# Kernel tuning notes

Measured on AMD Instinct MI355X. Metric: run time of the kernel, lower is better.

Reference implementation:

```python
import jax, jax.numpy as jnp
import numpy as np

D_MODEL = 1024
NUM_HEADS = 16
HEAD_DIM = D_MODEL // NUM_HEADS
B, S = 2, 2048


def setup_inputs() -> dict:
    key = jax.random.key(0)
    ks = jax.random.split(key, 6)
    scale = 0.02
    return {
        "x": jax.random.normal(ks[0], (B, S, D_MODEL), dtype=jnp.float32),
        "mask": jax.random.normal(ks[1], (S, S), dtype=jnp.float32),
        "Wqkv": jax.random.normal(ks[2], (D_MODEL, 3 * D_MODEL), dtype=jnp.float32) * scale,
        "bqkv": jax.random.normal(ks[3], (3 * D_MODEL,), dtype=jnp.float32) * scale,
        "Wout": jax.random.normal(ks[4], (D_MODEL, D_MODEL), dtype=jnp.float32) * scale,
        "bout": jax.random.normal(ks[5], (D_MODEL,), dtype=jnp.float32) * scale,
    }


def reference(x, mask, Wqkv, bqkv, Wout, bout):
    b, s, d = x.shape
    h, hd = NUM_HEADS, HEAD_DIM
    qkv = x @ Wqkv + bqkv                              # [b, s, 3d]
    qkv = qkv.reshape(b, s, h, 3 * hd).transpose(0, 2, 1, 3)  # [b, h, s, 3hd]
    q, k, v = jnp.split(qkv, 3, axis=-1)               # each [b, h, s, hd]
    scaled = jnp.einsum("bhqd,bhkd->bhqk", q, k) / jnp.sqrt(jnp.float32(hd))
    scaled = scaled + mask                             # mask [s, s] broadcasts
    attn = jax.nn.softmax(scaled, axis=-1)
    values = jnp.einsum("bhqk,bhkd->bhqd", attn, v)    # [b, h, s, hd]
    values = values.transpose(0, 2, 1, 3).reshape(b, s, d)
    return values @ Wout + bout
```

## Files before the change

### kernel.cpp

```cpp
#include <hip/hip_runtime.h>
#include <hip/hip_bf16.h>

#define D_MODEL 1024
#define NH 16
#define HD 64
#define BATCH 2
#define SEQ 2048
#define M_TOTAL (BATCH*SEQ)

typedef _Float16 f16;
typedef _Float16 half8 __attribute__((ext_vector_type(8)));
typedef _Float16 half4v __attribute__((ext_vector_type(4)));
typedef float floatx4 __attribute__((ext_vector_type(4)));

__device__ inline void gload_lds16(const void* g, void* l) {
    __builtin_amdgcn_global_load_lds(
        (const __attribute__((address_space(1))) unsigned int*)g,
        (__attribute__((address_space(3))) unsigned int*)l, 16, 0, 0);
}

__global__ void cvt_f32_f16(const float* __restrict__ src, f16* __restrict__ dst, int n4) {
    int i = blockIdx.x * blockDim.x + threadIdx.x;
    if (i < n4) {
        float4 v = ((const float4*)src)[i];
        half4v o = { (f16)v.x, (f16)v.y, (f16)v.z, (f16)v.w };
        *(half4v*)(dst + (long)i * 4) = o;
    }
}

__global__ void exp_cvt(const float* __restrict__ src, f16* __restrict__ dst, int n4) {
    int i = blockIdx.x * blockDim.x + threadIdx.x;
    if (i < n4) {
        float4 v = ((const float4*)src)[i];
        half4v o = { (f16)__expf(v.x), (f16)__expf(v.y), (f16)__expf(v.z), (f16)__expf(v.w) };
        *(half4v*)(dst + (long)i * 4) = o;
    }
}

__global__ void transpose_cvt(const float* __restrict__ src, f16* __restrict__ dst, int R, int C) {
    __shared__ float tile[32][33];
    int tx = threadIdx.x;
    int ty = threadIdx.y;
    int c0 = blockIdx.x * 32;
    int r0 = blockIdx.y * 32;
    for (int yy = 0; yy < 32; yy += 8)
        tile[ty + yy][tx] = src[(long)(r0 + ty + yy) * C + c0 + tx];
    __syncthreads();
    for (int yy = 0; yy < 32; yy += 8)
        dst[(long)(c0 + ty + yy) * R + r0 + tx] = (f16)tile[tx][ty + yy];
}

template<int MODE, int TN>
__global__ __launch_bounds__(256) void gemm_mfma(
    const f16* __restrict__ A, const f16* __restrict__ BT,
    const float* __restrict__ bias,
    f16* __restrict__ Qh, f16* __restrict__ Kh, f16* __restrict__ Vtg,
    float* __restrict__ out, int Kdim)
{
    constexpr int NF = TN / 32;
    __shared__ f16 Ah[128 * 64];
    __shared__ f16 Bh[TN * 64];
    int tid  = threadIdx.x;
    int wid  = tid >> 6;
    int lane = tid & 63;
    int quad = lane >> 4;
    int l16  = lane & 15;
    int m0 = blockIdx.y * 128;
    int n0 = blockIdx.x * TN;
    int mrow = (wid >> 1) * 64;
    int ncol = (wid & 1) * (TN / 2);
    int grow = lane >> 3;
    int gchunk = (lane & 7) ^ (grow & 7);
    int sw0 = ((quad)     ^ (l16 & 7)) * 8;
    int sw1 = ((quad + 4) ^ (l16 & 7)) * 8;

    floatx4 acc[4][NF];
    #pragma unroll
    for (int mb = 0; mb < 4; mb++)
        #pragma unroll
        for (int nb = 0; nb < NF; nb++) acc[mb][nb] = (floatx4){0.f, 0.f, 0.f, 0.f};

    const f16* Abase = A + (long)m0 * Kdim;
    const f16* Bbase = BT + (long)n0 * Kdim;

    for (int k0 = 0; k0 < Kdim; k0 += 64) {
        #pragma unroll
        for (int j = 0; j < 4; j++) {
            int r = j * 32 + wid * 8 + grow;
            gload_lds16(Abase + (long)r * Kdim + k0 + gchunk * 8, &Ah[(j * 32 + wid * 8) * 64]);
        }
        #pragma unroll
        for (int j = 0; j < TN / 32; j++) {
            int r = j * 32 + wid * 8 + grow;
            gload_lds16(Bbase + (long)r * Kdim + k0 + gchunk * 8, &Bh[(j * 32 + wid * 8) * 64]);
        }
        __syncthreads();
        #pragma unroll
        for (int h = 0; h < 2; h++) {
            int sw = h ? sw1 : sw0;
            half8 af[4];
            #pragma unroll
            for (int mb = 0; mb < 4; mb++)
                af[mb] = *(const half8*)&Ah[(mrow + mb * 16 + l16) * 64 + sw];
            #pragma unroll
            for (int nb = 0; nb < NF; nb++) {
                half8 bf = *(const half8*)&Bh[(ncol + nb * 16 + l16) * 64 + sw];
                #pragma unroll
                for (int mb = 0; mb < 4; mb++)
                    acc[mb][nb] = __builtin_amdgcn_mfma_f32_16x16x32_f16(af[mb], bf, acc[mb][nb], 0, 0, 0);
            }
        }
        __syncthreads();
    }

    #pragma unroll
    for (int nb = 0; nb < NF; nb++) {
        int n = n0 + ncol + nb * 16 + l16;
        float bv = bias[n];
        int head = 0, t = 0, d = 0;
        if (MODE == 0) { head = n / 192; int rem = n % 192; t = rem / 64; d = rem % 64; }
        #pragma unroll
        for (int mb = 0; mb < 4; mb++) {
            int mbase = m0 + mrow + mb * 16 + quad * 4;
            if (MODE == 0) {
                int b = mbase >> 11;
                int s = mbase & 2047;
                long bh = b * NH + head;
                if (t == 2) {
                    half4v pack;
                    #pragma unroll
                    for (int r = 0; r < 4; r++) pack[r] = (f16)(acc[mb][nb][r] + bv);
                    *(half4v*)&Vtg[(bh * HD + d) * SEQ + s] = pack;
                } else if (t == 0) {
                    #pragma unroll
                    for (int r = 0; r < 4; r++)
                        Qh[(bh * SEQ + s + r) * HD + d] = (f16)((acc[mb][nb][r] + bv) * 0.125f);
                } else {
                    #pragma unroll
                    for (int r = 0; r < 4; r++)
                        Kh[(bh * SEQ + s + r) * HD + d] = (f16)(acc[mb][nb][r] + bv);
                }
            } else {
                #pragma unroll
                for (int r = 0; r < 4; r++)
                    out[(long)(mbase + r) * D_MODEL + n] = acc[mb][nb][r] + bv;
            }
        }
    }
}

__global__ __launch_bounds__(256) void attn(
    const f16* __restrict__ Qh, const f16* __restrict__ Kh, const f16* __restrict__ Vtg,
    const f16* __restrict__ E, f16* __restrict__ valh)
{
    __shared__ f16 Kl[2][64 * 64];
    __shared__ f16 Vt[2][64 * 64];
    __shared__ f16 Pl[4][32 * 64];
    int tid  = threadIdx.x;
    int wid  = tid >> 6;
    int lane = tid & 63;
    int quad = lane >> 4;
    int l16  = lane & 15;
    int bh = blockIdx.y;
    int b  = bh >> 4;
    int h  = bh & 15;
    int q0 = blockIdx.x * 128 + wid * 32;

    int grow = lane >> 3;
    int gpos = lane & 7;
    int sw0 = ((quad)     ^ (l16 & 7)) * 8;
    int sw1 = ((quad + 4) ^ (l16 & 7)) * 8;

    const f16* Qbase = Qh + ((long)bh * SEQ + q0) * HD;
    half8 qf[2][2];
    #pragma unroll
    for (int m = 0; m < 2; m++)
        #pragma unroll
        for (int c = 0; c < 2; c++)
            qf[m][c] = *(const half8*)&Qbase[(long)(m * 16 + l16) * HD + c * 32 + quad * 8];

    half8 vones;
    #pragma unroll
    for (int j = 0; j < 8; j++) vones[j] = (f16)1.0f;

    floatx4 Of[2][4];
    floatx4 Ofs[2];
    #pragma unroll
    for (int m = 0; m < 2; m++) {
        Ofs[m] = (floatx4){0.f, 0.f, 0.f, 0.f};
        #pragma unroll
        for (int nb = 0; nb < 4; nb++) Of[m][nb] = (floatx4){0.f, 0.f, 0.f, 0.f};
    }

    const f16* Kb = Kh + (long)bh * SEQ * HD;
    const f16* Vb = Vtg + (long)bh * HD * SEQ;

    #pragma unroll
    for (int j = 0; j < 2; j++) {
        int rb = j * 32 + wid * 8;
        int row = rb + grow;
        int gk = gpos ^ (row & 7);
        gload_lds16(Kb + (long)row * HD + gk * 8, &Kl[0][rb * 64]);
        gload_lds16(Vb + (long)row * SEQ + gk * 8, &Vt[0][rb * 64]);
    }

    for (int it = 0; it < SEQ / 64; it++) {
        int cur = it & 1;
        int k0 = it * 64;
        __syncthreads();

        if (it < SEQ / 64 - 1) {
            int kn = k0 + 64;
            #pragma unroll
            for (int j = 0; j < 2; j++) {
                int rb = j * 32 + wid * 8;
                int row = rb + grow;
                int gk = gpos ^ (row & 7);
                gload_lds16(Kb + (long)(kn + row) * HD + gk * 8, &Kl[cur ^ 1][rb * 64]);
                gload_lds16(Vb + (long)row * SEQ + kn + gk * 8, &Vt[cur ^ 1][rb * 64]);
            }
        }

        half4v ef[2][4];
        #pragma unroll
        for (int m = 0; m < 2; m++)
            #pragma unroll
            for (int kb = 0; kb < 4; kb++)
                ef[m][kb] = *(const half4v*)&E[(long)(q0 + m * 16 + l16) * SEQ + k0 + kb * 16 + quad * 4];

        #pragma unroll
        for (int kb = 0; kb < 4; kb++) {
            half8 kf0 = *(const half8*)&Kl[cur][(kb * 16 + l16) * 64 + sw0];
            half8 kf1 = *(const half8*)&Kl[cur][(kb * 16 + l16) * 64 + sw1];
            #pragma unroll
            for (int m = 0; m < 2; m++) {
                floatx4 s = (floatx4){0.f, 0.f, 0.f, 0.f};
                s = __builtin_amdgcn_mfma_f32_16x16x32_f16(kf0, qf[m][0], s, 0, 0, 0);
                s = __builtin_amdgcn_mfma_f32_16x16x32_f16(kf1, qf[m][1], s, 0, 0, 0);
                half4v ph;
                #pragma unroll
                for (int r = 0; r < 4; r++)
                    ph[r] = (f16)((float)ef[m][kb][r] * __expf(s[r]));
                int c8 = ((kb * 2 + (quad >> 1)) ^ (l16 & 7)) * 8 + (quad & 1) * 4;
                *(half4v*)&Pl[wid][(m * 16 + l16) * 64 + c8] = ph;
            }
        }

        half8 pf[2][2];
        #pragma unroll
        for (int m = 0; m < 2; m++)
            #pragma unroll
            for (int c = 0; c < 2; c++) {
                int c8 = ((c * 4 + quad) ^ (l16 & 7)) * 8;
                pf[m][c] = *(const half8*)&Pl[wid][(m * 16 + l16) * 64 + c8];
            }

        #pragma unroll
        for (int nb = 0; nb < 4; nb++) {
            half8 vf0 = *(const half8*)&Vt[cur][(nb * 16 + l16) * 64 + sw0];
            half8 vf1 = *(const half8*)&Vt[cur][(nb * 16 + l16) * 64 + sw1];
            #pragma unroll
            for (int m = 0; m < 2; m++) {
                Of[m][nb] = __builtin_amdgcn_mfma_f32_16x16x32_f16(pf[m][0], vf0, Of[m][nb], 0, 0, 0);
                Of[m][nb] = __builtin_amdgcn_mfma_f32_16x16x32_f16(pf[m][1], vf1, Of[m][nb], 0, 0, 0);
            }
        }
        #pragma unroll
        for (int m = 0; m < 2; m++) {
            Ofs[m] = __builtin_amdgcn_mfma_f32_16x16x32_f16(pf[m][0], vones, Ofs[m], 0, 0, 0);
            Ofs[m] = __builtin_amdgcn_mfma_f32_16x16x32_f16(pf[m][1], vones, Ofs[m], 0, 0, 0);
        }
    }

    #pragma unroll
    for (int m = 0; m < 2; m++) {
        floatx4 rs;
        #pragma unroll
        for (int r = 0; r < 4; r++) rs[r] = 1.f / Ofs[m][r];
        #pragma unroll
        for (int nb = 0; nb < 4; nb++)
            #pragma unroll
            for (int r = 0; r < 4; r++) {
                int q = q0 + m * 16 + quad * 4 + r;
                int d = nb * 16 + l16;
                valh[((long)(b * SEQ + q)) * D_MODEL + h * HD + d] = (f16)(Of[m][nb][r] * rs[r]);
            }
    }
}

extern "C" void kernel_launch(void* const* d_in, const int* in_sizes, int n_in,
                              void* d_out, int out_size, void* d_ws, size_t ws_size,
                              hipStream_t stream) {
    const float* x    = (const float*)d_in[0];
    const float* mask = (const float*)d_in[1];
    const float* Wqkv = (const float*)d_in[2];
    const float* bqkv = (const float*)d_in[3];
    const float* Wout = (const float*)d_in[4];
    const float* bout = (const float*)d_in[5];
    float* out = (float*)d_out;

    char* ws = (char*)d_ws;
    f16* xh    = (f16*)(ws + 0);
    f16* E     = (f16*)(ws + 0);
    f16* WqkvT = (f16*)(ws + 8388608);
    f16* WoutT = (f16*)(ws + 14680064);
    f16* Qh    = (f16*)(ws + 16777216);
    f16* Kh    = (f16*)(ws + 25165824);
    f16* Vtg   = (f16*)(ws + 33554432);
    f16* valh  = (f16*)(ws + 41943040);

    cvt_f32_f16<<<4096, 256, 0, stream>>>(x, xh, M_TOTAL * D_MODEL / 4);
    transpose_cvt<<<dim3(96, 32), dim3(32, 8), 0, stream>>>(Wqkv, WqkvT, 1024, 3072);
    transpose_cvt<<<dim3(32, 32), dim3(32, 8), 0, stream>>>(Wout, WoutT, 1024, 1024);
    gemm_mfma<0, 128><<<dim3(24, 32), 256, 0, stream>>>(xh, WqkvT, bqkv, Qh, Kh, Vtg, nullptr, 1024);
    exp_cvt<<<4096, 256, 0, stream>>>(mask, E, SEQ * SEQ / 4);
    attn<<<dim3(16, 32), 256, 0, stream>>>(Qh, Kh, Vtg, E, valh);
    gemm_mfma<1, 64><<<dim3(16, 32), 256, 0, stream>>>(valh, WoutT, bout, nullptr, nullptr, nullptr, out, 1024);
}
```

Before: 259.1 us.

## Keep P in registers, feed PV via 16x16x16 MFMA, prefetch mask

Result: faster. 243.3 us (-6.1%).

```diff
diff --git a/kernel.cpp b/kernel.cpp
--- a/kernel.cpp
+++ b/kernel.cpp
@@ -155,7 +155,6 @@
 {
     __shared__ f16 Kl[2][64 * 64];
     __shared__ f16 Vt[2][64 * 64];
-    __shared__ f16 Pl[4][32 * 64];
     int tid  = threadIdx.x;
     int wid  = tid >> 6;
     int lane = tid & 63;
@@ -168,8 +167,11 @@
 
     int grow = lane >> 3;
     int gpos = lane & 7;
-    int sw0 = ((quad)     ^ (l16 & 7)) * 8;
-    int sw1 = ((quad + 4) ^ (l16 & 7)) * 8;
+    int l3   = l16 & 7;
+    int sw0 = ((quad)     ^ l3) * 8;
+    int sw1 = ((quad + 4) ^ l3) * 8;
+    int qh  = quad >> 1;
+    int ql4 = (quad & 1) * 4;
 
     const f16* Qbase = Qh + ((long)bh * SEQ + q0) * HD;
     half8 qf[2][2];
@@ -179,18 +181,12 @@
         for (int c = 0; c < 2; c++)
             qf[m][c] = *(const half8*)&Qbase[(long)(m * 16 + l16) * HD + c * 32 + quad * 8];
 
-    half8 vones;
-    #pragma unroll
-    for (int j = 0; j < 8; j++) vones[j] = (f16)1.0f;
-
     floatx4 Of[2][4];
-    floatx4 Ofs[2];
-    #pragma unroll
-    for (int m = 0; m < 2; m++) {
-        Ofs[m] = (floatx4){0.f, 0.f, 0.f, 0.f};
+    float sums[2] = {0.f, 0.f};
+    #pragma unroll
+    for (int m = 0; m < 2; m++)
         #pragma unroll
         for (int nb = 0; nb < 4; nb++) Of[m][nb] = (floatx4){0.f, 0.f, 0.f, 0.f};
-    }
 
     const f16* Kb = Kh + (long)bh * SEQ * HD;
     const f16* Vb = Vtg + (long)bh * HD * SEQ;
@@ -204,87 +200,87 @@
         gload_lds16(Vb + (long)row * SEQ + gk * 8, &Vt[0][rb * 64]);
     }
 
-    for (int it = 0; it < SEQ / 64; it++) {
-        int cur = it & 1;
-        int k0 = it * 64;
-        __syncthreads();
-
-        if (it < SEQ / 64 - 1) {
-            int kn = k0 + 64;
-            #pragma unroll
-            for (int j = 0; j < 2; j++) {
-                int rb = j * 32 + wid * 8;
-                int row = rb + grow;
-                int gk = gpos ^ (row & 7);
-                gload_lds16(Kb + (long)(kn + row) * HD + gk * 8, &Kl[cur ^ 1][rb * 64]);
-                gload_lds16(Vb + (long)row * SEQ + kn + gk * 8, &Vt[cur ^ 1][rb * 64]);
-            }
-        }
-
-        half4v ef[2][4];
-        #pragma unroll
-        for (int m = 0; m < 2; m++)
-            #pragma unroll
-            for (int kb = 0; kb < 4; kb++)
-                ef[m][kb] = *(const half4v*)&E[(long)(q0 + m * 16 + l16) * SEQ + k0 + kb * 16 + quad * 4];
-
-        #pragma unroll
-        for (int kb = 0; kb < 4; kb++) {
-            half8 kf0 = *(const half8*)&Kl[cur][(kb * 16 + l16) * 64 + sw0];
-            half8 kf1 = *(const half8*)&Kl[cur][(kb * 16 + l16) * 64 + sw1];
-            #pragma unroll
-            for (int m = 0; m < 2; m++) {
-                floatx4 s = (floatx4){0.f, 0.f, 0.f, 0.f};
-                s = __builtin_amdgcn_mfma_f32_16x16x32_f16(kf0, qf[m][0], s, 0, 0, 0);
-                s = __builtin_amdgcn_mfma_f32_16x16x32_f16(kf1, qf[m][1], s, 0, 0, 0);
-                half4v ph;
-                #pragma unroll
-                for (int r = 0; r < 4; r++)
-                    ph[r] = (f16)((float)ef[m][kb][r] * __expf(s[r]));
-                int c8 = ((kb * 2 + (quad >> 1)) ^ (l16 & 7)) * 8 + (quad & 1) * 4;
-                *(half4v*)&Pl[wid][(m * 16 + l16) * 64 + c8] = ph;
-            }
-        }
-
-        half8 pf[2][2];
-        #pragma unroll
-        for (int m = 0; m < 2; m++)
-            #pragma unroll
-            for (int c = 0; c < 2; c++) {
-                int c8 = ((c * 4 + quad) ^ (l16 & 7)) * 8;
-                pf[m][c] = *(const half8*)&Pl[wid][(m * 16 + l16) * 64 + c8];
-            }
-
+    half4v ef[2][2][4];
+    #pragma unroll
+    for (int m = 0; m < 2; m++)
+        #pragma unroll
+        for (int kb = 0; kb < 4; kb++)
+            ef[0][m][kb] = *(const half4v*)&E[(long)(q0 + m * 16 + l16) * SEQ + kb * 16 + quad * 4];
+
+    for (int it2 = 0; it2 < SEQ / 128; it2++) {
+        #pragma unroll
+        for (int p = 0; p < 2; p++) {
+            int k0 = it2 * 128 + p * 64;
+            __syncthreads();
+
+            if (k0 + 64 < SEQ) {
+                int kn = k0 + 64;
+                #pragma unroll
+                for (int j = 0; j < 2; j++) {
+                    int rb = j * 32 + wid * 8;
+                    int row = rb + grow;
+                    int gk = gpos ^ (row & 7);
+                    gload_lds16(Kb + (long)(kn + row) * HD + gk * 8, &Kl[p ^ 1][rb * 64]);
+                    gload_lds16(Vb + (long)row * SEQ + kn + gk * 8, &Vt[p ^ 1][rb * 64]);
+                }
+                #pragma unroll
+                for (int m = 0; m < 2; m++)
+                    #pragma unroll
+                    for (int kb = 0; kb < 4; kb++)
+                        ef[p ^ 1][m][kb] = *(const half4v*)&E[(long)(q0 + m * 16 + l16) * SEQ + kn + kb * 16 + quad * 4];
+            }
+
+            half4v ph[2][4];
+            #pragma unroll
+            for (int kb = 0; kb < 4; kb++) {
+                half8 kf0 = *(const half8*)&Kl[p][(kb * 16 + l16) * 64 + sw0];
+                half8 kf1 = *(const half8*)&Kl[p][(kb * 16 + l16) * 64 + sw1];
+                #pragma unroll
+                for (int m = 0; m < 2; m++) {
+                    floatx4 s = (floatx4){0.f, 0.f, 0.f, 0.f};
+                    s = __builtin_amdgcn_mfma_f32_16x16x32_f16(kf0, qf[m][0], s, 0, 0, 0);
+                    s = __builtin_amdgcn_mfma_f32_16x16x32_f16(kf1, qf[m][1], s, 0, 0, 0);
+                    #pragma unroll
+                    for (int r = 0; r < 4; r++) {
+                        float pv = (float)ef[p][m][kb][r] * __expf(s[r]);
+                        sums[m] += pv;
+                        ph[m][kb][r] = (f16)pv;
+                    }
+                }
+            }
+
+            #pragma unroll
+            for (int kb = 0; kb < 4; kb++) {
+                int chunk = ((kb * 2 + qh) ^ l3) * 8 + ql4;
+                #pragma unroll
+                for (int nb = 0; nb < 4; nb++) {
+                    half4v vf = *(const half4v*)&Vt[p][(nb * 16 + l16) * 64 + chunk];
+                    #pragma unroll
+                    for (int m = 0; m < 2; m++)
+                        Of[m][nb] = __builtin_amdgcn_mfma_f32_16x16x16f16(vf, ph[m][kb], Of[m][nb], 0, 0, 0);
+                }
+            }
+        }
+    }
+
+    #pragma unroll
+    for (int m = 0; m < 2; m++) {
+        float s = sums[m];
+        s += __shfl_xor(s, 16);
+        s += __shfl_xor(s, 32);
+        sums[m] = 1.f / s;
+    }
+
+    #pragma unroll
+    for (int m = 0; m < 2; m++) {
+        long row = (long)(b * SEQ + q0 + m * 16 + l16) * D_MODEL + h * HD;
         #pragma unroll
         for (int nb = 0; nb < 4; nb++) {
-            half8 vf0 = *(const half8*)&Vt[cur][(nb * 16 + l16) * 64 + sw0];
-            half8 vf1 = *(const half8*)&Vt[cur][(nb * 16 + l16) * 64 + sw1];
-            #pragma unroll
-            for (int m = 0; m < 2; m++) {
-                Of[m][nb] = __builtin_amdgcn_mfma_f32_16x16x32_f16(pf[m][0], vf0, Of[m][nb], 0, 0, 0);
-                Of[m][nb] = __builtin_amdgcn_mfma_f32_16x16x32_f16(pf[m][1], vf1, Of[m][nb], 0, 0, 0);
-            }
-        }
-        #pragma unroll
-        for (int m = 0; m < 2; m++) {
-            Ofs[m] = __builtin_amdgcn_mfma_f32_16x16x32_f16(pf[m][0], vones, Ofs[m], 0, 0, 0);
-            Ofs[m] = __builtin_amdgcn_mfma_f32_16x16x32_f16(pf[m][1], vones, Ofs[m], 0, 0, 0);
-        }
-    }
-
-    #pragma unroll
-    for (int m = 0; m < 2; m++) {
-        floatx4 rs;
-        #pragma unroll
-        for (int r = 0; r < 4; r++) rs[r] = 1.f / Ofs[m][r];
-        #pragma unroll
-        for (int nb = 0; nb < 4; nb++)
-            #pragma unroll
-            for (int r = 0; r < 4; r++) {
-                int q = q0 + m * 16 + quad * 4 + r;
-                int d = nb * 16 + l16;
-                valh[((long)(b * SEQ + q)) * D_MODEL + h * HD + d] = (f16)(Of[m][nb][r] * rs[r]);
-            }
+            half4v o;
+            #pragma unroll
+            for (int r = 0; r < 4; r++) o[r] = (f16)(Of[m][nb][r] * sums[m]);
+            *(half4v*)&valh[row + nb * 16 + quad * 4] = o;
+        }
     }
 }
 
```
